# Kernel optimization log

Measured on AMD Instinct MI355X. Metric: run time of the kernel, lower is better.

The kernel has to match this reference:

```python
import jax, jax.numpy as jnp
import numpy as np

KERNEL = 4
STRIDE = 2
PADDING = 1


def setup_inputs() -> dict:
    key = jax.random.key(0)
    k1, k2, k3 = jax.random.split(key, 3)
    x = jax.random.normal(k1, (256, 128, 128), dtype=jnp.float32)
    W = jax.random.normal(k2, (128, 256, KERNEL, KERNEL), dtype=jnp.float32) * 0.02
    b = jax.random.normal(k3, (128,), dtype=jnp.float32) * 0.02
    return {"x": x, "W": W, "b": b}


def reference(x, W, b):
    # Original: zero-insert x with stride 2 (at[:, ::2].set), pad by
    # (kernel - padding - 1) on each spatial side, then dense stride-1 conv.
    # lhs_dilation=STRIDE performs the identical zero-insertion (size 2H-1)
    # without materializing the sparse intermediate; padding matches jnp.pad.
    pad = KERNEL - PADDING - 1  # = 2
    out = jax.lax.conv_general_dilated(
        x[None],  # (1, C_in, H, W)
        W,        # (C_out, C_in, k, k), cross-correlation as in equinox Conv2d
        window_strides=(1, 1),
        padding=((pad, pad), (pad, pad)),
        lhs_dilation=(STRIDE, STRIDE),
        dimension_numbers=("NCHW", "OIHW", "NCHW"),
    )[0]
    return out + b[:, None, None]
```

## Files before the change

kernel.cpp:

```cpp
#include <hip/hip_runtime.h>


typedef __attribute__((ext_vector_type(8))) short bf16x8;
typedef __attribute__((ext_vector_type(16))) float f32x16;

#define CI 256
#define CO 128
#define HW 128
#define YO_TILE 4
#define XO_TILE 16
#define CELLS_R 6
#define CELLS_C 18
#define NCELLS (CELLS_R * CELLS_C)
#define LDS_BYTES (NCELLS * 512)

static __device__ __forceinline__ unsigned short f2bf(float f) {
  union { float f; unsigned u; } v; v.f = f;
  return (unsigned short)((v.u + 0x7FFFu + ((v.u >> 16) & 1u)) >> 16);
}

__global__ __launch_bounds__(256) void transpose_x_kernel(const float* __restrict__ x,
                                                          unsigned short* __restrict__ xbT) {
  __shared__ unsigned short tileT[64][68];
  const int hw0 = blockIdx.x * 64;
  const int ci0 = blockIdx.y * 64;
  const int tid = threadIdx.x;
#pragma unroll
  for (int it = 0; it < 4; ++it) {
    const int p = it * 256 + tid;
    const int ci_r = p >> 4;
    const int c4 = p & 15;
    const float4 v = *(const float4*)(x + (size_t)(ci0 + ci_r) * (HW * HW) + hw0 + c4 * 4);
    tileT[c4 * 4 + 0][ci_r] = f2bf(v.x);
    tileT[c4 * 4 + 1][ci_r] = f2bf(v.y);
    tileT[c4 * 4 + 2][ci_r] = f2bf(v.z);
    tileT[c4 * 4 + 3][ci_r] = f2bf(v.w);
  }
  __syncthreads();
#pragma unroll
  for (int it = 0; it < 2; ++it) {
    const int p = it * 256 + tid;
    const int cg = p & 7;
    const int hw = p >> 3;
    const bf16x8 v = *(const bf16x8*)&tileT[hw][cg * 8];
    *(bf16x8*)(xbT + (size_t)(hw0 + hw) * CI + ci0 + cg * 8) = v;
  }
}

__global__ __launch_bounds__(256) void reorg_w_kernel(const float* __restrict__ W,
                                                      unsigned short* __restrict__ Wb) {
  const int tid = blockIdx.x * 256 + threadIdx.x;
  const int f = tid * 4;
  const int tap0 = f & 15;
  const int ci = (f >> 4) & 255;
  const int o = f >> 12;
  const float4 v = *(const float4*)(W + f);
  const int base = ((ci >> 4) * CO + o) * 16 + (ci & 15);
  Wb[(tap0 + 0) * 32768 + base] = f2bf(v.x);
  Wb[(tap0 + 1) * 32768 + base] = f2bf(v.y);
  Wb[(tap0 + 2) * 32768 + base] = f2bf(v.z);
  Wb[(tap0 + 3) * 32768 + base] = f2bf(v.w);
}

__global__ __launch_bounds__(1024, 4) void tconv_mfma_kernel(
    const unsigned short* __restrict__ xbT,
    const unsigned short* __restrict__ Wb,
    const float* __restrict__ bias,
    float* __restrict__ out) {
  __shared__ __align__(16) unsigned char LDS[LDS_BYTES];
  const int tid = threadIdx.x;
  const int X0 = blockIdx.x * XO_TILE;
  const int Y0 = blockIdx.y * YO_TILE;

  for (int e = tid; e < NCELLS * 32; e += 1024) {
    const int s = e & 31;
    const int cell = e >> 5;
    const int c = cell % CELLS_C;
    const int r = cell / CELLS_C;
    const int gr = Y0 - 1 + r;
    const int gc = X0 - 1 + c;
    uint4 val = make_uint4(0u, 0u, 0u, 0u);
    if (gr >= 0 && gr < HW && gc >= 0 && gc < HW)
      val = *(const uint4*)(xbT + ((gr * HW + gc) * CI + s * 8));
    *(uint4*)(LDS + cell * 512 + ((s ^ c) * 16)) = val;
  }
  __syncthreads();

  const int lane = tid & 63;
  const int wave = tid >> 6;
  const int cls = wave & 3;
  const int ry = cls >> 1, rx = cls & 1;
  const int mh = (wave >> 2) & 1;
  const int sph = wave >> 3;
  const int l31 = lane & 31;
  const int lhi = lane >> 5;
  const int nrow = l31 >> 4;
  const int ncol = l31 & 15;

  f32x16 acc[2];
#pragma unroll
  for (int mt = 0; mt < 2; ++mt)
#pragma unroll
    for (int t = 0; t < 16; ++t) acc[mt][t] = 0.0f;

#pragma unroll
  for (int a = 0; a < 2; ++a) {
#pragma unroll
    for (int b = 0; b < 2; ++b) {
      const int tap = (2 * a + ry) * 4 + (2 * b + rx);
      const int c_l = ncol + rx + b;
      const int r_base = sph * 2 + nrow + ry + a;
      const int cellbase = (r_base * CELLS_C + c_l) * 512;
      const unsigned short* wt = Wb + tap * 32768 + (mh * 64 + l31) * 16 + lhi * 8;
#pragma unroll
      for (int cb = 0; cb < 16; ++cb) {
        const int s_idx = cb * 2 + lhi;
        const bf16x8 bfrag = *(const bf16x8*)(LDS + cellbase + ((s_idx ^ c_l) * 16));
        const unsigned short* wk = wt + cb * 2048;
#pragma unroll
        for (int mt = 0; mt < 2; ++mt)
          acc[mt] = __builtin_amdgcn_mfma_f32_32x32x16_bf16(
              *(const bf16x8*)(wk + mt * 512), bfrag, acc[mt], 0, 0, 0);
      }
    }
  }

  const int yo = Y0 + sph * 2 + nrow;
  const int xo = X0 + ncol;
  const int y = 2 * yo + ry;
  const int xg = 2 * xo + rx;
#pragma unroll
  for (int mt = 0; mt < 2; ++mt)
#pragma unroll
    for (int t = 0; t < 16; ++t) {
      const int rowD = (t & 3) + 4 * lhi + 8 * (t >> 2);
      const int o = mh * 64 + mt * 32 + rowD;
      out[((size_t)o << 16) + (y << 8) + xg] = acc[mt][t] + bias[o];
    }
}

extern "C" void kernel_launch(void* const* d_in, const int* in_sizes, int n_in,
                              void* d_out, int out_size, void* d_ws, size_t ws_size,
                              hipStream_t stream) {
  const float* x = (const float*)d_in[0];
  const float* W = (const float*)d_in[1];
  const float* b = (const float*)d_in[2];
  float* out = (float*)d_out;

  unsigned short* xbT = (unsigned short*)d_ws;
  unsigned short* Wb = xbT + (size_t)CI * HW * HW;

  transpose_x_kernel<<<dim3((HW * HW) / 64, CI / 64), dim3(256), 0, stream>>>(x, xbT);
  reorg_w_kernel<<<dim3(512), dim3(256), 0, stream>>>(W, Wb);
  tconv_mfma_kernel<<<dim3(HW / XO_TILE, HW / YO_TILE), dim3(1024), 0, stream>>>(xbT, Wb, b, out);
}
```

Baseline: 108.2 us.

## Split output channels across grid and register-block each wave over two spatial tiles

The conv kernel now uses 256-thread blocks over 8x8 output tiles, with the output-channel half taken from blockIdx.z instead of the wave index. Each wave now holds a 2x2 set of MFMA accumulators, so each weight fragment load feeds two spatial tiles and each LDS fragment feeds two channel tiles. This cuts global weight traffic per MFMA and gives more independent MFMAs per iteration. In exchange the input halo (10x10 cells) is loaded twice, once per channel half, and the larger accumulator set raises register pressure.

```diff
diff --git a/kernel.cpp b/kernel.cpp
--- a/kernel.cpp
+++ b/kernel.cpp
@@ -7,10 +7,10 @@
 #define CI 256
 #define CO 128
 #define HW 128
-#define YO_TILE 4
-#define XO_TILE 16
-#define CELLS_R 6
-#define CELLS_C 18
+#define YO_TILE 8
+#define XO_TILE 8
+#define CELLS_R 10
+#define CELLS_C 10
 #define NCELLS (CELLS_R * CELLS_C)
 #define LDS_BYTES (NCELLS * 512)
 
@@ -62,7 +62,7 @@
   Wb[(tap0 + 3) * 32768 + base] = f2bf(v.w);
 }
 
-__global__ __launch_bounds__(1024, 4) void tconv_mfma_kernel(
+__global__ __launch_bounds__(256, 2) void tconv_mfma_kernel(
     const unsigned short* __restrict__ xbT,
     const unsigned short* __restrict__ Wb,
     const float* __restrict__ bias,
@@ -71,8 +71,9 @@
   const int tid = threadIdx.x;
   const int X0 = blockIdx.x * XO_TILE;
   const int Y0 = blockIdx.y * YO_TILE;
+  const int mh = blockIdx.z;
 
-  for (int e = tid; e < NCELLS * 32; e += 1024) {
+  for (int e = tid; e < NCELLS * 32; e += 256) {
     const int s = e & 31;
     const int cell = e >> 5;
     const int c = cell % CELLS_C;
@@ -87,21 +88,20 @@
   __syncthreads();
 
   const int lane = tid & 63;
-  const int wave = tid >> 6;
-  const int cls = wave & 3;
+  const int cls = tid >> 6;
   const int ry = cls >> 1, rx = cls & 1;
-  const int mh = (wave >> 2) & 1;
-  const int sph = wave >> 3;
   const int l31 = lane & 31;
   const int lhi = lane >> 5;
-  const int nrow = l31 >> 4;
-  const int ncol = l31 & 15;
+  const int nrow = l31 >> 3;
+  const int ncol = l31 & 7;
 
-  f32x16 acc[2];
+  f32x16 acc[2][2];
 #pragma unroll
   for (int mt = 0; mt < 2; ++mt)
 #pragma unroll
-    for (int t = 0; t < 16; ++t) acc[mt][t] = 0.0f;
+    for (int nt = 0; nt < 2; ++nt)
+#pragma unroll
+      for (int t = 0; t < 16; ++t) acc[mt][nt][t] = 0.0f;
 
 #pragma unroll
   for (int a = 0; a < 2; ++a) {
@@ -109,33 +109,40 @@
     for (int b = 0; b < 2; ++b) {
       const int tap = (2 * a + ry) * 4 + (2 * b + rx);
       const int c_l = ncol + rx + b;
-      const int r_base = sph * 2 + nrow + ry + a;
-      const int cellbase = (r_base * CELLS_C + c_l) * 512;
+      const int r0 = nrow + ry + a;
+      const int cellbase0 = (r0 * CELLS_C + c_l) * 512;
+      const int cellbase1 = ((r0 + 4) * CELLS_C + c_l) * 512;
       const unsigned short* wt = Wb + tap * 32768 + (mh * 64 + l31) * 16 + lhi * 8;
 #pragma unroll
       for (int cb = 0; cb < 16; ++cb) {
-        const int s_idx = cb * 2 + lhi;
-        const bf16x8 bfrag = *(const bf16x8*)(LDS + cellbase + ((s_idx ^ c_l) * 16));
+        const int off = ((cb * 2 + lhi) ^ c_l) * 16;
+        const bf16x8 bf0 = *(const bf16x8*)(LDS + cellbase0 + off);
+        const bf16x8 bf1 = *(const bf16x8*)(LDS + cellbase1 + off);
         const unsigned short* wk = wt + cb * 2048;
-#pragma unroll
-        for (int mt = 0; mt < 2; ++mt)
-          acc[mt] = __builtin_amdgcn_mfma_f32_32x32x16_bf16(
-              *(const bf16x8*)(wk + mt * 512), bfrag, acc[mt], 0, 0, 0);
+        const bf16x8 af0 = *(const bf16x8*)(wk);
+        const bf16x8 af1 = *(const bf16x8*)(wk + 512);
+        acc[0][0] = __builtin_amdgcn_mfma_f32_32x32x16_bf16(af0, bf0, acc[0][0], 0, 0, 0);
+        acc[0][1] = __builtin_amdgcn_mfma_f32_32x32x16_bf16(af0, bf1, acc[0][1], 0, 0, 0);
+        acc[1][0] = __builtin_amdgcn_mfma_f32_32x32x16_bf16(af1, bf0, acc[1][0], 0, 0, 0);
+        acc[1][1] = __builtin_amdgcn_mfma_f32_32x32x16_bf16(af1, bf1, acc[1][1], 0, 0, 0);
       }
     }
   }
 
-  const int yo = Y0 + sph * 2 + nrow;
   const int xo = X0 + ncol;
-  const int y = 2 * yo + ry;
   const int xg = 2 * xo + rx;
 #pragma unroll
   for (int mt = 0; mt < 2; ++mt)
 #pragma unroll
-    for (int t = 0; t < 16; ++t) {
-      const int rowD = (t & 3) + 4 * lhi + 8 * (t >> 2);
-      const int o = mh * 64 + mt * 32 + rowD;
-      out[((size_t)o << 16) + (y << 8) + xg] = acc[mt][t] + bias[o];
+    for (int nt = 0; nt < 2; ++nt) {
+      const int yo = Y0 + nt * 4 + nrow;
+      const int y = 2 * yo + ry;
+#pragma unroll
+      for (int t = 0; t < 16; ++t) {
+        const int rowD = (t & 3) + 4 * lhi + 8 * (t >> 2);
+        const int o = mh * 64 + mt * 32 + rowD;
+        out[((size_t)o << 16) + (y << 8) + xg] = acc[mt][nt][t] + bias[o];
+      }
     }
 }
 
@@ -152,5 +159,5 @@
 
   transpose_x_kernel<<<dim3((HW * HW) / 64, CI / 64), dim3(256), 0, stream>>>(x, xbT);
   reorg_w_kernel<<<dim3(512), dim3(256), 0, stream>>>(W, Wb);
-  tconv_mfma_kernel<<<dim3(HW / XO_TILE, HW / YO_TILE), dim3(1024), 0, stream>>>(xbT, Wb, b, out);
+  tconv_mfma_kernel<<<dim3(HW / XO_TILE, HW / YO_TILE, 2), dim3(256), 0, stream>>>(xbT, Wb, b, out);
 }
```

Result: no change. 109.1 us (+0.7%).
